# Kernel tuning notes

Hardware: AMD Instinct MI355X
Metric: run time of the kernel (lower is better)

Reference implementation:

```python
import jax, jax.numpy as jnp
import numpy as np

G, S, M = 4, 2048, 1024   # groups (batch), tokens per group, emb dim
E, H, K = 8, 4096, 2      # experts, mlp dim, top-k
CAP = int(K * S / E * 1.25)  # expert capacity = 640
AUX_COEF, Z_COEF = 0.01, 0.001


def setup_inputs() -> dict:
    key = jax.random.key(0)
    k1, k2, k3, k4, k5 = jax.random.split(key, 5)
    return {
        "inputs": jax.random.normal(k1, (G, S, M), jnp.float32),
        "paddings": jnp.zeros((G, S), jnp.float32),  # 1.0 = padded token
        "router_w": jax.random.normal(k2, (M, E), jnp.float32) / np.sqrt(M),
        "wi_gate": jax.random.normal(k3, (E, M, H), jnp.float32) / np.sqrt(M),
        "wi_0": jax.random.normal(k4, (E, M, H), jnp.float32) / np.sqrt(M),
        "wo": jax.random.normal(k5, (E, H, M), jnp.float32) / np.sqrt(H),
    }


def reference(inputs, paddings, router_w, wi_gate, wi_0, wo):
    # Router
    logits = jnp.einsum('gsm,me->gse', inputs, router_w)          # [G,S,E]
    probs = jax.nn.softmax(logits, axis=-1)
    top_p, top_i = jax.lax.top_k(probs, K)                        # [G,S,K]

    nonpad = 1.0 - paddings                                       # [G,S]
    exp_mask = jax.nn.one_hot(top_i, E, dtype=jnp.float32)        # [G,S,K,E]
    exp_mask = exp_mask * nonpad[:, :, None, None]

    # Position in expert (capacity-limited), priority by token order then k slot
    mask_flat = exp_mask.reshape(G, S * K, E)
    pos = jnp.cumsum(mask_flat, axis=1) * mask_flat               # 1-indexed where assigned
    keep = mask_flat * (pos <= CAP)
    pos_oh = jax.nn.one_hot((pos - 1.0).astype(jnp.int32), CAP, dtype=jnp.float32)  # [G,SK,E,CAP]
    dispatch_k = (keep[..., None] * pos_oh).reshape(G, S, K, E, CAP)
    dispatch = dispatch_k.sum(axis=2)                             # [G,S,E,CAP]
    combine = jnp.einsum('gsk,gskec->gsec', top_p, dispatch_k)    # [G,S,E,CAP]

    # Dispatch -> gated expert FFN -> combine
    expert_in = jnp.einsum('gsec,gsm->egcm', dispatch, inputs)    # [E,G,CAP,M]
    h = jax.nn.silu(jnp.einsum('egcm,emh->egch', expert_in, wi_gate)) \
        * jnp.einsum('egcm,emh->egch', expert_in, wi_0)           # [E,G,CAP,H]
    expert_out = jnp.einsum('egch,ehm->egcm', h, wo)              # [E,G,CAP,M]
    output = jnp.einsum('gsec,egcm->gsm', combine, expert_out)    # [G,S,M]

    # Aux losses: load-balancing (Switch style) + router z-loss
    em = jnp.max(jax.nn.one_hot(top_i, E, dtype=jnp.float32), axis=-2)       # [G,S,E]
    lb = jnp.mean(jnp.mean(em, axis=-2) * jnp.mean(probs, axis=-2)) * E * E
    z = jnp.mean(jax.nn.logsumexp(logits, axis=-1) ** 2)
    aux_loss = AUX_COEF * lb + Z_COEF * z
    return output, aux_loss
```

## Files before the change

### kernel.cpp

```cpp
#include <hip/hip_runtime.h>
#include <hip/hip_bf16.h>
#include <math.h>

#define G 4
#define S 2048
#define MDIM 1024
#define E 8
#define HDIM 4096
#define TOPK 2
#define CAP 640
#define GC (G*CAP)

typedef __attribute__((ext_vector_type(8))) short bf16x8;
typedef __attribute__((ext_vector_type(4))) short s16x4;
typedef __attribute__((ext_vector_type(4))) float f32x4;
typedef unsigned int u32;
typedef unsigned short u16;

#define MFMA16(a,b,c) __builtin_amdgcn_mfma_f32_16x16x32_bf16(a,b,c,0,0,0)

__device__ __forceinline__ u16 f2bf(float f) {
    union { float f; u32 u; } v; v.f = f;
    u32 r = v.u + 0x7fffu + ((v.u >> 16) & 1u);
    return (u16)(r >> 16);
}

__device__ __forceinline__ void gload16(const char* gp, char* lp) {
    __builtin_amdgcn_global_load_lds((const __attribute__((address_space(1))) u32*)gp,
                                     (__attribute__((address_space(3))) u32*)lp,
                                     16, 0, 0);
}

__device__ __forceinline__ int swzb(int r) { return ((r >> 1) & 3) << 4; }

__global__ __launch_bounds__(256) void transpose_cvt(const float* __restrict__ in,
                                                     u16* __restrict__ out, int R, int C) {
    int e = blockIdx.z;
    const float* ine = in + (size_t)e * R * C;
    u16* oute = out + (size_t)e * R * C;
    __shared__ float tile[64][68];
    int t = threadIdx.x;
    int x0 = blockIdx.x * 64, y0 = blockIdx.y * 64;
    int lx = (t & 15) * 4, ly = t >> 4;
    #pragma unroll
    for (int i = 0; i < 4; ++i) {
        f32x4 v = *(const f32x4*)(ine + (size_t)(y0 + ly + i * 16) * C + x0 + lx);
        *(f32x4*)&tile[ly + i * 16][lx] = v;
    }
    __syncthreads();
    int rr0 = (t & 15) * 4, cb = t >> 4;
    #pragma unroll
    for (int p = 0; p < 4; ++p) {
        int cc = cb + p * 16;
        s16x4 pk;
        #pragma unroll
        for (int j = 0; j < 4; ++j) pk[j] = (short)f2bf(tile[rr0 + j][cc]);
        *(s16x4*)(oute + (size_t)(x0 + cc) * R + y0 + rr0) = pk;
    }
}

__global__ __launch_bounds__(256) void router_kernel(const float* __restrict__ inp,
                                                     const float* __restrict__ rw,
                                                     int* __restrict__ top_i,
                                                     float* __restrict__ top_p,
                                                     float* __restrict__ partials) {
    int wid = threadIdx.x >> 6, lane = threadIdx.x & 63;
    int tok = blockIdx.x * 4 + wid;
    const float* x = inp + (size_t)tok * MDIM;
    float acc[E] = {0.f,0.f,0.f,0.f,0.f,0.f,0.f,0.f};
    #pragma unroll
    for (int rep = 0; rep < 4; ++rep) {
        int m0 = rep * 256 + lane * 4;
        f32x4 xv = *(const f32x4*)(x + m0);
        #pragma unroll
        for (int j = 0; j < 4; ++j) {
            const float* r = rw + (size_t)(m0 + j) * E;
            float xj = xv[j];
            #pragma unroll
            for (int e = 0; e < E; ++e) acc[e] += xj * r[e];
        }
    }
    #pragma unroll
    for (int e = 0; e < E; ++e)
        #pragma unroll
        for (int off = 32; off; off >>= 1) acc[e] += __shfl_down(acc[e], off);

    __shared__ float part[4][17];
    if (lane == 0) {
        float mx = acc[0];
        #pragma unroll
        for (int e = 1; e < E; ++e) mx = fmaxf(mx, acc[e]);
        float p[E], sum = 0.f;
        #pragma unroll
        for (int e = 0; e < E; ++e) { p[e] = expf(acc[e] - mx); sum += p[e]; }
        float inv = 1.f / sum;
        #pragma unroll
        for (int e = 0; e < E; ++e) p[e] *= inv;
        float lse = logf(sum) + mx;
        int i0 = 0;
        #pragma unroll
        for (int e = 1; e < E; ++e) if (acc[e] > acc[i0]) i0 = e;
        int i1 = (i0 == 0) ? 1 : 0;
        #pragma unroll
        for (int e = 0; e < E; ++e) if (e != i0 && acc[e] > acc[i1]) i1 = e;
        top_i[tok*2+0] = i0; top_i[tok*2+1] = i1;
        top_p[tok*2+0] = p[i0]; top_p[tok*2+1] = p[i1];
        #pragma unroll
        for (int e = 0; e < E; ++e) { part[wid][e] = p[e]; part[wid][8+e] = 0.f; }
        part[wid][8+i0] = 1.f; part[wid][8+i1] = 1.f;
        part[wid][16] = lse * lse;
    }
    __syncthreads();
    if (threadIdx.x < 17) {
        float v = part[0][threadIdx.x] + part[1][threadIdx.x] +
                  part[2][threadIdx.x] + part[3][threadIdx.x];
        partials[(size_t)blockIdx.x * 17 + threadIdx.x] = v;
    }
}

__global__ __launch_bounds__(256) void reduce_partials(const float* __restrict__ partials,
                                                       float* __restrict__ sums) {
    int g = blockIdx.x, t = threadIdx.x;
    float loc[17];
    #pragma unroll
    for (int c = 0; c < 17; ++c) loc[c] = 0.f;
    for (int r = t; r < 1024; r += 256) {
        const float* pr = partials + ((size_t)g * 1024 + r) * 17;
        #pragma unroll
        for (int c = 0; c < 17; ++c) loc[c] += pr[c];
    }
    __shared__ float red[256];
    for (int c = 0; c < 17; ++c) {
        red[t] = loc[c]; __syncthreads();
        for (int off = 128; off; off >>= 1) {
            if (t < off) red[t] += red[t + off];
            __syncthreads();
        }
        if (t == 0) sums[g * 17 + c] = red[0];
        __syncthreads();
    }
}

__global__ void aux_final(const float* __restrict__ sums, float* __restrict__ out) {
    float lb = 0.f, z = 0.f;
    for (int g = 0; g < G; ++g) {
        for (int e = 0; e < E; ++e)
            lb += (sums[g*17 + 8 + e] / (float)S) * (sums[g*17 + e] / (float)S);
        z += sums[g*17 + 16];
    }
    lb = lb / (float)(G * E) * (float)(E * E);
    z /= (float)(G * S);
    out[(size_t)G * S * MDIM] = 0.01f * lb + 0.001f * z;
}

__global__ __launch_bounds__(256) void scan_kernel(const int* __restrict__ top_i,
                                                   const float* __restrict__ pad,
                                                   int* __restrict__ slot_token,
                                                   int* __restrict__ token_c) {
    int b = blockIdx.x; int g = b >> 3, e = b & 7;
    int t = threadIdx.x;
    __shared__ int sums[256];
    int base = t * 16;
    int run = 0; unsigned mask16 = 0; int loc[16];
    #pragma unroll
    for (int j = 0; j < 16; ++j) {
        int i = base + j; int s = i >> 1, k = i & 1;
        int ex = top_i[((size_t)(g * S + s)) * 2 + k];
        int m = (ex == e) && (pad[g * S + s] == 0.f);
        run += m; loc[j] = run; mask16 |= ((unsigned)m << j);
    }
    sums[t] = run; __syncthreads();
    for (int off = 1; off < 256; off <<= 1) {
        int v = (t >= off) ? sums[t - off] : 0;
        __syncthreads();
        sums[t] += v;
        __syncthreads();
    }
    int excl = sums[t] - run;
    #pragma unroll
    for (int j = 0; j < 16; ++j) {
        if ((mask16 >> j) & 1u) {
            int pos = excl + loc[j];
            if (pos <= CAP) {
                int i = base + j; int s = i >> 1, k = i & 1;
                slot_token[((size_t)(e * G + g)) * CAP + (pos - 1)] = s;
                token_c[((size_t)(g * S + s)) * 2 + k] = pos - 1;
            }
        }
    }
}

__global__ __launch_bounds__(128) void gather_kernel(const float* __restrict__ inp,
                                                     const int* __restrict__ slot_token,
                                                     u16* __restrict__ X) {
    int row = blockIdx.x;
    int t = threadIdx.x;
    int s = slot_token[row];
    int g = (row % GC) / CAP;
    bf16x8 v;
    if (s >= 0) {
        const float* src = inp + ((size_t)(g * S + s)) * MDIM + t * 8;
        f32x4 a = *(const f32x4*)src;
        f32x4 b = *(const f32x4*)(src + 4);
        #pragma unroll
        for (int j = 0; j < 4; ++j) { v[j] = (short)f2bf(a[j]); v[4+j] = (short)f2bf(b[j]); }
    } else {
        #pragma unroll
        for (int j = 0; j < 8; ++j) v[j] = 0;
    }
    *(bf16x8*)(X + (size_t)row * MDIM + t * 8) = v;
}

__global__ __launch_bounds__(256, 2) void gemm_ffn12_v6(
        const u16* __restrict__ Xb, const u16* __restrict__ WgT,
        const u16* __restrict__ W0T, u16* __restrict__ Hb) {
    extern __shared__ char smem[];
    const int NK = MDIM / 32;
    int bid = blockIdx.x;
    int swz = (bid & 7) * 640 + (bid >> 3);
    int mt = swz % 20, nt = (swz / 20) % 32, e = swz / 640;
    const char* A  = (const char*)(Xb  + (size_t)e * GC * MDIM   + (size_t)mt * 128 * MDIM);
    const char* Bg = (const char*)(WgT + (size_t)e * HDIM * MDIM + (size_t)nt * 128 * MDIM);
    const char* B0 = (const char*)(W0T + (size_t)e * HDIM * MDIM + (size_t)nt * 128 * MDIM);
    int tid = threadIdx.x, w = tid >> 6, l = tid & 63;
    int wm = w >> 1, wn = w & 1;
    int rl = l >> 2, cch = (l & 3) * 16;
    int fr = l & 15, fg = l >> 4;
    int lswz = ((fr >> 1) & 3) << 4;

    int r0 = 0 * 64 + w * 16 + rl, r1 = 1 * 64 + w * 16 + rl;
    const char* gA0 = A  + (size_t)r0 * MDIM * 2 + (cch ^ swzb(r0));
    const char* gA1 = A  + (size_t)r1 * MDIM * 2 + (cch ^ swzb(r1));
    const char* gG0 = Bg + (size_t)r0 * MDIM * 2 + (cch ^ swzb(r0));
    const char* gG1 = Bg + (size_t)r1 * MDIM * 2 + (cch ^ swzb(r1));
    const char* gO0 = B0 + (size_t)r0 * MDIM * 2 + (cch ^ swzb(r0));
    const char* gO1 = B0 + (size_t)r1 * MDIM * 2 + (cch ^ swzb(r1));
    int baseA = (wm * 64 + fr) * 64 + ((fg * 16) ^ lswz);
    int baseB = (wn * 64 + fr) * 64 + ((fg * 16) ^ lswz);

    f32x4 ag[4][4], ao[4][4];
    #pragma unroll
    for (int i = 0; i < 4; ++i)
        #pragma unroll
        for (int j = 0; j < 4; ++j) { ag[i][j] = (f32x4){0,0,0,0}; ao[i][j] = (f32x4){0,0,0,0}; }

    auto stage = [&](int tt) {
        int kk = tt * 64;
        char* dst = smem + (tt & 1) * 24576;
        gload16(gA0 + kk, dst + 0 * 4096 + w * 1024);
        gload16(gA1 + kk, dst + 1 * 4096 + w * 1024);
        gload16(gG0 + kk, dst + 8192 + 0 * 4096 + w * 1024);
        gload16(gG1 + kk, dst + 8192 + 1 * 4096 + w * 1024);
        gload16(gO0 + kk, dst + 16384 + 0 * 4096 + w * 1024);
        gload16(gO1 + kk, dst + 16384 + 1 * 4096 + w * 1024);
    };

    stage(0);
    asm volatile("s_waitcnt vmcnt(0)" ::: "memory");
    __builtin_amdgcn_s_barrier();

    #pragma unroll 1
    for (int t = 0; t < NK; ++t) {
        if (t + 1 < NK) stage(t + 1);
        const char* bufc = smem + (t & 1) * 24576;
        bf16x8 af[4], bg_[4], bo_[4];
        #pragma unroll
        for (int fm = 0; fm < 4; ++fm) af[fm]  = *(const bf16x8*)(bufc + baseA + fm * 1024);
        #pragma unroll
        for (int fn = 0; fn < 4; ++fn) bg_[fn] = *(const bf16x8*)(bufc + 8192  + baseB + fn * 1024);
        #pragma unroll
        for (int fn = 0; fn < 4; ++fn) bo_[fn] = *(const bf16x8*)(bufc + 16384 + baseB + fn * 1024);
        __builtin_amdgcn_s_setprio(1);
        #pragma unroll
        for (int fm = 0; fm < 4; ++fm)
            #pragma unroll
            for (int fn = 0; fn < 4; ++fn) {
                ag[fm][fn] = MFMA16(bg_[fn], af[fm], ag[fm][fn]);
                ao[fm][fn] = MFMA16(bo_[fn], af[fm], ao[fm][fn]);
            }
        __builtin_amdgcn_s_setprio(0);
        asm volatile("s_waitcnt vmcnt(0)" ::: "memory");
        __builtin_amdgcn_s_barrier();
    }

    u16* He = Hb + (size_t)e * GC * HDIM;
    int row0 = mt * 128 + wm * 64 + fr;
    int col0 = nt * 128 + wn * 64 + fg * 4;
    #pragma unroll
    for (int fm = 0; fm < 4; ++fm)
        #pragma unroll
        for (int fn = 0; fn < 4; ++fn) {
            s16x4 pk;
            #pragma unroll
            for (int r = 0; r < 4; ++r) {
                float gv = ag[fm][fn][r], ov = ao[fm][fn][r];
                float hv = gv / (1.f + __expf(-gv)) * ov;
                pk[r] = (short)f2bf(hv);
            }
            *(s16x4*)(He + (size_t)(row0 + fm * 16) * HDIM + col0 + fn * 16) = pk;
        }
}

__global__ __launch_bounds__(256, 2) void gemm_out_v6(
        const u16* __restrict__ Hb, const u16* __restrict__ WoT,
        float* __restrict__ EO) {
    extern __shared__ char smem[];
    const int NK = HDIM / 32;
    int bid = blockIdx.x;
    int swz = (bid & 7) * 80 + (bid >> 3);
    int mt = swz % 20, nt = (swz / 20) & 3, e = swz / 80;
    const char* A = (const char*)(Hb  + (size_t)e * GC * HDIM   + (size_t)mt * 128 * HDIM);
    const char* B = (const char*)(WoT + (size_t)e * MDIM * HDIM + (size_t)nt * 256 * HDIM);
    int tid = threadIdx.x, w = tid >> 6, l = tid & 63;
    int wm = w >> 1, wn = w & 1;
    int rl = l >> 2, cch = (l & 3) * 16;
    int fr = l & 15, fg = l >> 4;
    int lswz = ((fr >> 1) & 3) << 4;

    int r0 = 0 * 64 + w * 16 + rl, r1 = 1 * 64 + w * 16 + rl;
    int r2 = 2 * 64 + w * 16 + rl, r3 = 3 * 64 + w * 16 + rl;
    const char* gA0 = A + (size_t)r0 * HDIM * 2 + (cch ^ swzb(r0));
    const char* gA1 = A + (size_t)r1 * HDIM * 2 + (cch ^ swzb(r1));
    const char* gB0 = B + (size_t)r0 * HDIM * 2 + (cch ^ swzb(r0));
    const char* gB1 = B + (size_t)r1 * HDIM * 2 + (cch ^ swzb(r1));
    const char* gB2 = B + (size_t)r2 * HDIM * 2 + (cch ^ swzb(r2));
    const char* gB3 = B + (size_t)r3 * HDIM * 2 + (cch ^ swzb(r3));
    int baseA = (wm * 64  + fr) * 64 + ((fg * 16) ^ lswz);
    int baseB = (wn * 128 + fr) * 64 + ((fg * 16) ^ lswz);

    f32x4 acc[4][8];
    #pragma unroll
    for (int i = 0; i < 4; ++i)
        #pragma unroll
        for (int j = 0; j < 8; ++j) acc[i][j] = (f32x4){0,0,0,0};

    auto stage = [&](int tt) {
        int kk = tt * 64;
        char* dst = smem + (tt & 1) * 24576;
        gload16(gA0 + kk, dst + 0 * 4096 + w * 1024);
        gload16(gA1 + kk, dst + 1 * 4096 + w * 1024);
        gload16(gB0 + kk, dst + 8192 + 0 * 4096 + w * 1024);
        gload16(gB1 + kk, dst + 8192 + 1 * 4096 + w * 1024);
        gload16(gB2 + kk, dst + 8192 + 2 * 4096 + w * 1024);
        gload16(gB3 + kk, dst + 8192 + 3 * 4096 + w * 1024);
    };

    stage(0);
    asm volatile("s_waitcnt vmcnt(0)" ::: "memory");
    __builtin_amdgcn_s_barrier();

    #pragma unroll 1
    for (int t = 0; t < NK; ++t) {
        if (t + 1 < NK) stage(t + 1);
        const char* bufc = smem + (t & 1) * 24576;
        bf16x8 af[4], bf[8];
        #pragma unroll
        for (int fm = 0; fm < 4; ++fm) af[fm] = *(const bf16x8*)(bufc + baseA + fm * 1024);
        #pragma unroll
        for (int fn = 0; fn < 8; ++fn) bf[fn] = *(const bf16x8*)(bufc + 8192 + baseB + fn * 1024);
        __builtin_amdgcn_s_setprio(1);
        #pragma unroll
        for (int fm = 0; fm < 4; ++fm)
            #pragma unroll
            for (int fn = 0; fn < 8; ++fn)
                acc[fm][fn] = MFMA16(bf[fn], af[fm], acc[fm][fn]);
        __builtin_amdgcn_s_setprio(0);
        asm volatile("s_waitcnt vmcnt(0)" ::: "memory");
        __builtin_amdgcn_s_barrier();
    }

    float* Ee = EO + (size_t)e * GC * MDIM;
    int row0 = mt * 128 + wm * 64 + fr;
    int col0 = nt * 256 + wn * 128 + fg * 4;
    #pragma unroll
    for (int fm = 0; fm < 4; ++fm)
        #pragma unroll
        for (int fn = 0; fn < 8; ++fn)
            *(f32x4*)(Ee + (size_t)(row0 + fm * 16) * MDIM + col0 + fn * 16) = acc[fm][fn];
}

__global__ __launch_bounds__(256) void combine_kernel(const float* __restrict__ EO,
                                                      const int* __restrict__ top_i,
                                                      const float* __restrict__ top_p,
                                                      const int* __restrict__ token_c,
                                                      float* __restrict__ out) {
    int tok = blockIdx.x, t = threadIdx.x;
    int g = tok >> 11;
    f32x4 acc = {0.f, 0.f, 0.f, 0.f};
    #pragma unroll
    for (int k = 0; k < 2; ++k) {
        int c = token_c[tok * 2 + k];
        if (c >= 0) {
            int e = top_i[tok * 2 + k];
            float p = top_p[tok * 2 + k];
            const float* src = EO + ((size_t)e * GC + g * CAP + c) * MDIM + t * 4;
            f32x4 v = *(const f32x4*)src;
            #pragma unroll
            for (int j = 0; j < 4; ++j) acc[j] += p * v[j];
        }
    }
    *(f32x4*)(out + (size_t)tok * MDIM + t * 4) = acc;
}

extern "C" void kernel_launch(void* const* d_in, const int* in_sizes, int n_in,
                              void* d_out, int out_size, void* d_ws, size_t ws_size,
                              hipStream_t stream) {
    (void)in_sizes; (void)n_in; (void)out_size; (void)ws_size;
    const float* inputs   = (const float*)d_in[0];
    const float* paddings = (const float*)d_in[1];
    const float* router_w = (const float*)d_in[2];
    const float* wi_gate  = (const float*)d_in[3];
    const float* wi_0     = (const float*)d_in[4];
    const float* wo       = (const float*)d_in[5];
    float* out = (float*)d_out;

    char* p = (char*)d_ws;
    u16* WgT = (u16*)p; p += (size_t)E * HDIM * MDIM * 2;
    u16* W0T = (u16*)p; p += (size_t)E * HDIM * MDIM * 2;
    u16* WoT = (u16*)p; p += (size_t)E * HDIM * MDIM * 2;
    u16* Xb  = (u16*)p; p += (size_t)E * GC * MDIM * 2;
    u16* Hb  = (u16*)p; p += (size_t)E * GC * HDIM * 2;
    float* EO = (float*)p; p += (size_t)E * GC * MDIM * 4;
    int*   top_i = (int*)p;   p += (size_t)G * S * TOPK * 4;
    float* top_p = (float*)p; p += (size_t)G * S * TOPK * 4;
    int*   token_c = (int*)p; p += (size_t)G * S * TOPK * 4;
    int*   slot_token = (int*)p; p += (size_t)E * G * CAP * 4;
    float* partials = (float*)p; p += (size_t)4096 * 17 * 4;
    float* sums = (float*)p; p += 4 * 17 * 4;

    hipMemsetAsync(token_c, 0xFF, (size_t)G * S * TOPK * 4, stream);
    hipMemsetAsync(slot_token, 0xFF, (size_t)E * G * CAP * 4, stream);

    hipFuncSetAttribute((const void*)gemm_ffn12_v6,
                        hipFuncAttributeMaxDynamicSharedMemorySize, 49152);
    hipFuncSetAttribute((const void*)gemm_out_v6,
                        hipFuncAttributeMaxDynamicSharedMemorySize, 49152);

    transpose_cvt<<<dim3(HDIM/64, MDIM/64, E), 256, 0, stream>>>(wi_gate, WgT, MDIM, HDIM);
    transpose_cvt<<<dim3(HDIM/64, MDIM/64, E), 256, 0, stream>>>(wi_0,   W0T, MDIM, HDIM);
    transpose_cvt<<<dim3(MDIM/64, HDIM/64, E), 256, 0, stream>>>(wo,     WoT, HDIM, MDIM);

    router_kernel<<<G * S / 4, 256, 0, stream>>>(inputs, router_w, top_i, top_p, partials);
    reduce_partials<<<G, 256, 0, stream>>>(partials, sums);
    scan_kernel<<<G * E, 256, 0, stream>>>(top_i, paddings, slot_token, token_c);
    gather_kernel<<<E * GC, 128, 0, stream>>>(inputs, slot_token, Xb);
    gemm_ffn12_v6<<<5120, 256, 49152, stream>>>(Xb, WgT, W0T, Hb);
    gemm_out_v6<<<640, 256, 49152, stream>>>(Hb, WoT, EO);
    combine_kernel<<<G * S, 256, 0, stream>>>(EO, top_i, top_p, token_c, out);
    aux_final<<<1, 1, 0, stream>>>(sums, out);
}
```

Measured before the change: 802.8 us.

## Retile expert GEMMs to 512-thread blocks with 32x32x16 MFMA and K=64 stages

Both expert FFN GEMMs move from 256-thread blocks using 16x16x32 MFMA with K=32 LDS stages to 512-thread blocks using 32x32x16 MFMA with K=64 stages and a wider 128-byte XOR swizzle. The gate/up GEMM also grows its M tile from 128 to 256 rows, halving the grid and increasing reuse of weight tiles. The aim is fewer barriers per unit of work, fewer LDS reads per MFMA flop, and better operand reuse. In exchange, each block uses more LDS (up to 128 KB) and runs at one block per CU, which lowers occupancy and may reduce latency hiding.

```diff
diff --git a/kernel.cpp b/kernel.cpp
--- a/kernel.cpp
+++ b/kernel.cpp
@@ -14,10 +14,12 @@
 typedef __attribute__((ext_vector_type(8))) short bf16x8;
 typedef __attribute__((ext_vector_type(4))) short s16x4;
 typedef __attribute__((ext_vector_type(4))) float f32x4;
+typedef __attribute__((ext_vector_type(16))) float f32x16;
 typedef unsigned int u32;
 typedef unsigned short u16;
 
-#define MFMA16(a,b,c) __builtin_amdgcn_mfma_f32_16x16x32_bf16(a,b,c,0,0,0)
+#define MFMA32(a,b,c) __builtin_amdgcn_mfma_f32_32x32x16_bf16(a,b,c,0,0,0)
+#define BAR() __builtin_amdgcn_s_barrier()
 
 __device__ __forceinline__ u16 f2bf(float f) {
     union { float f; u32 u; } v; v.f = f;
@@ -31,7 +33,7 @@
                                      16, 0, 0);
 }
 
-__device__ __forceinline__ int swzb(int r) { return ((r >> 1) & 3) << 4; }
+__device__ __forceinline__ int swz128(int r) { return ((r >> 1) & 7) << 4; }
 
 __global__ __launch_bounds__(256) void transpose_cvt(const float* __restrict__ in,
                                                      u16* __restrict__ out, int R, int C) {
@@ -211,172 +213,212 @@
     *(bf16x8*)(X + (size_t)row * MDIM + t * 8) = v;
 }
 
-__global__ __launch_bounds__(256, 2) void gemm_ffn12_v6(
+__global__ __launch_bounds__(512, 1) void gemm_ffn12_v9(
         const u16* __restrict__ Xb, const u16* __restrict__ WgT,
         const u16* __restrict__ W0T, u16* __restrict__ Hb) {
     extern __shared__ char smem[];
-    const int NK = MDIM / 32;
+    const int NK = MDIM / 64;
     int bid = blockIdx.x;
-    int swz = (bid & 7) * 640 + (bid >> 3);
-    int mt = swz % 20, nt = (swz / 20) % 32, e = swz / 640;
-    const char* A  = (const char*)(Xb  + (size_t)e * GC * MDIM   + (size_t)mt * 128 * MDIM);
+    int swz = (bid & 7) * 320 + (bid >> 3);
+    int mt = swz % 10, nt = (swz / 10) & 31, e = swz / 320;
+    const char* A  = (const char*)(Xb  + (size_t)e * GC * MDIM   + (size_t)mt * 256 * MDIM);
     const char* Bg = (const char*)(WgT + (size_t)e * HDIM * MDIM + (size_t)nt * 128 * MDIM);
     const char* B0 = (const char*)(W0T + (size_t)e * HDIM * MDIM + (size_t)nt * 128 * MDIM);
     int tid = threadIdx.x, w = tid >> 6, l = tid & 63;
-    int wm = w >> 1, wn = w & 1;
-    int rl = l >> 2, cch = (l & 3) * 16;
-    int fr = l & 15, fg = l >> 4;
-    int lswz = ((fr >> 1) & 3) << 4;
-
-    int r0 = 0 * 64 + w * 16 + rl, r1 = 1 * 64 + w * 16 + rl;
-    const char* gA0 = A  + (size_t)r0 * MDIM * 2 + (cch ^ swzb(r0));
-    const char* gA1 = A  + (size_t)r1 * MDIM * 2 + (cch ^ swzb(r1));
-    const char* gG0 = Bg + (size_t)r0 * MDIM * 2 + (cch ^ swzb(r0));
-    const char* gG1 = Bg + (size_t)r1 * MDIM * 2 + (cch ^ swzb(r1));
-    const char* gO0 = B0 + (size_t)r0 * MDIM * 2 + (cch ^ swzb(r0));
-    const char* gO1 = B0 + (size_t)r1 * MDIM * 2 + (cch ^ swzb(r1));
-    int baseA = (wm * 64 + fr) * 64 + ((fg * 16) ^ lswz);
-    int baseB = (wn * 64 + fr) * 64 + ((fg * 16) ^ lswz);
-
-    f32x4 ag[4][4], ao[4][4];
-    #pragma unroll
-    for (int i = 0; i < 4; ++i)
-        #pragma unroll
-        for (int j = 0; j < 4; ++j) { ag[i][j] = (f32x4){0,0,0,0}; ao[i][j] = (f32x4){0,0,0,0}; }
+    int wm = w >> 2, wn = w & 3;
+    int lr = l & 31, lk = l >> 5;
+    int lswz = ((lr >> 1) & 7) << 4;
+
+    int koff[4];
+    #pragma unroll
+    for (int ks = 0; ks < 4; ++ks) koff[ks] = (ks * 32 + lk * 16) ^ lswz;
+    int baseA[4];
+    #pragma unroll
+    for (int rb = 0; rb < 4; ++rb) baseA[rb] = (wm * 128 + rb * 32 + lr) * 128;
+    int baseB = (wn * 32 + lr) * 128;
+
+    const char* srcA[4]; const char* srcG[2]; const char* srcO[2];
+    #pragma unroll
+    for (int p = 0; p < 4; ++p) {
+        int gr = p * 64 + w * 8 + (l >> 3);
+        srcA[p] = A + (size_t)gr * (MDIM * 2) + (((l & 7) * 16) ^ swz128(gr));
+    }
+    #pragma unroll
+    for (int p = 0; p < 2; ++p) {
+        int gr = p * 64 + w * 8 + (l >> 3);
+        srcG[p] = Bg + (size_t)gr * (MDIM * 2) + (((l & 7) * 16) ^ swz128(gr));
+        srcO[p] = B0 + (size_t)gr * (MDIM * 2) + (((l & 7) * 16) ^ swz128(gr));
+    }
+
+    f32x16 zz;
+    #pragma unroll
+    for (int i = 0; i < 16; ++i) zz[i] = 0.f;
+    f32x16 ag[4], ao[4];
+    #pragma unroll
+    for (int rb = 0; rb < 4; ++rb) { ag[rb] = zz; ao[rb] = zz; }
 
     auto stage = [&](int tt) {
-        int kk = tt * 64;
-        char* dst = smem + (tt & 1) * 24576;
-        gload16(gA0 + kk, dst + 0 * 4096 + w * 1024);
-        gload16(gA1 + kk, dst + 1 * 4096 + w * 1024);
-        gload16(gG0 + kk, dst + 8192 + 0 * 4096 + w * 1024);
-        gload16(gG1 + kk, dst + 8192 + 1 * 4096 + w * 1024);
-        gload16(gO0 + kk, dst + 16384 + 0 * 4096 + w * 1024);
-        gload16(gO1 + kk, dst + 16384 + 1 * 4096 + w * 1024);
+        int kk = tt * 128;
+        char* dst = smem + (tt & 1) * 65536;
+        #pragma unroll
+        for (int p = 0; p < 4; ++p)
+            gload16(srcA[p] + kk, dst + (p * 64 + w * 8) * 128);
+        #pragma unroll
+        for (int p = 0; p < 2; ++p) {
+            gload16(srcG[p] + kk, dst + 32768 + (p * 64 + w * 8) * 128);
+            gload16(srcO[p] + kk, dst + 49152 + (p * 64 + w * 8) * 128);
+        }
     };
 
     stage(0);
     asm volatile("s_waitcnt vmcnt(0)" ::: "memory");
-    __builtin_amdgcn_s_barrier();
+    BAR();
 
     #pragma unroll 1
     for (int t = 0; t < NK; ++t) {
         if (t + 1 < NK) stage(t + 1);
-        const char* bufc = smem + (t & 1) * 24576;
-        bf16x8 af[4], bg_[4], bo_[4];
-        #pragma unroll
-        for (int fm = 0; fm < 4; ++fm) af[fm]  = *(const bf16x8*)(bufc + baseA + fm * 1024);
-        #pragma unroll
-        for (int fn = 0; fn < 4; ++fn) bg_[fn] = *(const bf16x8*)(bufc + 8192  + baseB + fn * 1024);
-        #pragma unroll
-        for (int fn = 0; fn < 4; ++fn) bo_[fn] = *(const bf16x8*)(bufc + 16384 + baseB + fn * 1024);
-        __builtin_amdgcn_s_setprio(1);
-        #pragma unroll
-        for (int fm = 0; fm < 4; ++fm)
-            #pragma unroll
-            for (int fn = 0; fn < 4; ++fn) {
-                ag[fm][fn] = MFMA16(bg_[fn], af[fm], ag[fm][fn]);
-                ao[fm][fn] = MFMA16(bo_[fn], af[fm], ao[fm][fn]);
+        const char* bufc = smem + (t & 1) * 65536;
+        #pragma unroll
+        for (int ks = 0; ks < 4; ++ks) {
+            bf16x8 bg = *(const bf16x8*)(bufc + 32768 + baseB + koff[ks]);
+            bf16x8 bo = *(const bf16x8*)(bufc + 49152 + baseB + koff[ks]);
+            bf16x8 af[4];
+            #pragma unroll
+            for (int rb = 0; rb < 4; ++rb)
+                af[rb] = *(const bf16x8*)(bufc + baseA[rb] + koff[ks]);
+            __builtin_amdgcn_s_setprio(1);
+            #pragma unroll
+            for (int rb = 0; rb < 4; ++rb) {
+                ag[rb] = MFMA32(bg, af[rb], ag[rb]);
+                ao[rb] = MFMA32(bo, af[rb], ao[rb]);
             }
-        __builtin_amdgcn_s_setprio(0);
+            __builtin_amdgcn_s_setprio(0);
+        }
         asm volatile("s_waitcnt vmcnt(0)" ::: "memory");
-        __builtin_amdgcn_s_barrier();
+        BAR();
     }
 
     u16* He = Hb + (size_t)e * GC * HDIM;
-    int row0 = mt * 128 + wm * 64 + fr;
-    int col0 = nt * 128 + wn * 64 + fg * 4;
-    #pragma unroll
-    for (int fm = 0; fm < 4; ++fm)
-        #pragma unroll
-        for (int fn = 0; fn < 4; ++fn) {
+    int row0 = mt * 256 + wm * 128 + lr;
+    int col0 = nt * 128 + wn * 32 + lk * 4;
+    #pragma unroll
+    for (int rb = 0; rb < 4; ++rb) {
+        size_t rowoff = (size_t)(row0 + rb * 32) * HDIM;
+        #pragma unroll
+        for (int q = 0; q < 4; ++q) {
             s16x4 pk;
             #pragma unroll
             for (int r = 0; r < 4; ++r) {
-                float gv = ag[fm][fn][r], ov = ao[fm][fn][r];
+                float gv = ag[rb][q * 4 + r], ov = ao[rb][q * 4 + r];
                 float hv = gv / (1.f + __expf(-gv)) * ov;
                 pk[r] = (short)f2bf(hv);
             }
-            *(s16x4*)(He + (size_t)(row0 + fm * 16) * HDIM + col0 + fn * 16) = pk;
-        }
-}
-
-__global__ __launch_bounds__(256, 2) void gemm_out_v6(
+            *(s16x4*)(He + rowoff + col0 + q * 8) = pk;
+        }
+    }
+}
+
+__global__ __launch_bounds__(512, 1) void gemm_out_v9(
         const u16* __restrict__ Hb, const u16* __restrict__ WoT,
         float* __restrict__ EO) {
     extern __shared__ char smem[];
-    const int NK = HDIM / 32;
+    const int NK = HDIM / 64;
     int bid = blockIdx.x;
     int swz = (bid & 7) * 80 + (bid >> 3);
-    int mt = swz % 20, nt = (swz / 20) & 3, e = swz / 80;
+    int nt = swz & 3, mt = (swz / 4) % 20, e = swz / 80;
     const char* A = (const char*)(Hb  + (size_t)e * GC * HDIM   + (size_t)mt * 128 * HDIM);
     const char* B = (const char*)(WoT + (size_t)e * MDIM * HDIM + (size_t)nt * 256 * HDIM);
     int tid = threadIdx.x, w = tid >> 6, l = tid & 63;
-    int wm = w >> 1, wn = w & 1;
-    int rl = l >> 2, cch = (l & 3) * 16;
-    int fr = l & 15, fg = l >> 4;
-    int lswz = ((fr >> 1) & 3) << 4;
-
-    int r0 = 0 * 64 + w * 16 + rl, r1 = 1 * 64 + w * 16 + rl;
-    int r2 = 2 * 64 + w * 16 + rl, r3 = 3 * 64 + w * 16 + rl;
-    const char* gA0 = A + (size_t)r0 * HDIM * 2 + (cch ^ swzb(r0));
-    const char* gA1 = A + (size_t)r1 * HDIM * 2 + (cch ^ swzb(r1));
-    const char* gB0 = B + (size_t)r0 * HDIM * 2 + (cch ^ swzb(r0));
-    const char* gB1 = B + (size_t)r1 * HDIM * 2 + (cch ^ swzb(r1));
-    const char* gB2 = B + (size_t)r2 * HDIM * 2 + (cch ^ swzb(r2));
-    const char* gB3 = B + (size_t)r3 * HDIM * 2 + (cch ^ swzb(r3));
-    int baseA = (wm * 64  + fr) * 64 + ((fg * 16) ^ lswz);
-    int baseB = (wn * 128 + fr) * 64 + ((fg * 16) ^ lswz);
-
-    f32x4 acc[4][8];
-    #pragma unroll
-    for (int i = 0; i < 4; ++i)
-        #pragma unroll
-        for (int j = 0; j < 8; ++j) acc[i][j] = (f32x4){0,0,0,0};
+    int wm = w >> 2, wn = w & 3;
+    int lr = l & 31, lk = l >> 5;
+    int lswz = ((lr >> 1) & 7) << 4;
+
+    int koff[4];
+    #pragma unroll
+    for (int ks = 0; ks < 4; ++ks) koff[ks] = (ks * 32 + lk * 16) ^ lswz;
+    int baseA[2], baseB[2];
+    #pragma unroll
+    for (int rb = 0; rb < 2; ++rb) baseA[rb] = (wm * 64 + rb * 32 + lr) * 128;
+    #pragma unroll
+    for (int cb = 0; cb < 2; ++cb) baseB[cb] = (wn * 64 + cb * 32 + lr) * 128;
+
+    const char* srcA[2]; const char* srcB[4];
+    #pragma unroll
+    for (int p = 0; p < 2; ++p) {
+        int gr = p * 64 + w * 8 + (l >> 3);
+        srcA[p] = A + (size_t)gr * (HDIM * 2) + (((l & 7) * 16) ^ swz128(gr));
+    }
+    #pragma unroll
+    for (int p = 0; p < 4; ++p) {
+        int gr = p * 64 + w * 8 + (l >> 3);
+        srcB[p] = B + (size_t)gr * (HDIM * 2) + (((l & 7) * 16) ^ swz128(gr));
+    }
+
+    f32x16 zz;
+    #pragma unroll
+    for (int i = 0; i < 16; ++i) zz[i] = 0.f;
+    f32x16 acc[2][2];
+    #pragma unroll
+    for (int i = 0; i < 2; ++i)
+        #pragma unroll
+        for (int j = 0; j < 2; ++j) acc[i][j] = zz;
 
     auto stage = [&](int tt) {
-        int kk = tt * 64;
-        char* dst = smem + (tt & 1) * 24576;
-        gload16(gA0 + kk, dst + 0 * 4096 + w * 1024);
-        gload16(gA1 + kk, dst + 1 * 4096 + w * 1024);
-        gload16(gB0 + kk, dst + 8192 + 0 * 4096 + w * 1024);
-        gload16(gB1 + kk, dst + 8192 + 1 * 4096 + w * 1024);
-        gload16(gB2 + kk, dst + 8192 + 2 * 4096 + w * 1024);
-        gload16(gB3 + kk, dst + 8192 + 3 * 4096 + w * 1024);
+        int kk = tt * 128;
+        char* dst = smem + (tt & 1) * 49152;
+        #pragma unroll
+        for (int p = 0; p < 2; ++p)
+            gload16(srcA[p] + kk, dst + (p * 64 + w * 8) * 128);
+        #pragma unroll
+        for (int p = 0; p < 4; ++p)
+            gload16(srcB[p] + kk, dst + 16384 + (p * 64 + w * 8) * 128);
     };
 
     stage(0);
     asm volatile("s_waitcnt vmcnt(0)" ::: "memory");
-    __builtin_amdgcn_s_barrier();
+    BAR();
 
     #pragma unroll 1
     for (int t = 0; t < NK; ++t) {
         if (t + 1 < NK) stage(t + 1);
-        const char* bufc = smem + (t & 1) * 24576;
-        bf16x8 af[4], bf[8];
-        #pragma unroll
-        for (int fm = 0; fm < 4; ++fm) af[fm] = *(const bf16x8*)(bufc + baseA + fm * 1024);
-        #pragma unroll
-        for (int fn = 0; fn < 8; ++fn) bf[fn] = *(const bf16x8*)(bufc + 8192 + baseB + fn * 1024);
-        __builtin_amdgcn_s_setprio(1);
-        #pragma unroll
-        for (int fm = 0; fm < 4; ++fm)
-            #pragma unroll
-            for (int fn = 0; fn < 8; ++fn)
-                acc[fm][fn] = MFMA16(bf[fn], af[fm], acc[fm][fn]);
-        __builtin_amdgcn_s_setprio(0);
+        const char* bufc = smem + (t & 1) * 49152;
+        #pragma unroll
+        for (int ks = 0; ks < 4; ++ks) {
+            bf16x8 bf[2], af[2];
+            #pragma unroll
+            for (int cb = 0; cb < 2; ++cb)
+                bf[cb] = *(const bf16x8*)(bufc + 16384 + baseB[cb] + koff[ks]);
+            #pragma unroll
+            for (int rb = 0; rb < 2; ++rb)
+                af[rb] = *(const bf16x8*)(bufc + baseA[rb] + koff[ks]);
+            __builtin_amdgcn_s_setprio(1);
+            #pragma unroll
+            for (int rb = 0; rb < 2; ++rb)
+                #pragma unroll
+                for (int cb = 0; cb < 2; ++cb)
+                    acc[rb][cb] = MFMA32(bf[cb], af[rb], acc[rb][cb]);
+            __builtin_amdgcn_s_setprio(0);
+        }
         asm volatile("s_waitcnt vmcnt(0)" ::: "memory");
-        __builtin_amdgcn_s_barrier();
+        BAR();
     }
 
     float* Ee = EO + (size_t)e * GC * MDIM;
-    int row0 = mt * 128 + wm * 64 + fr;
-    int col0 = nt * 256 + wn * 128 + fg * 4;
-    #pragma unroll
-    for (int fm = 0; fm < 4; ++fm)
-        #pragma unroll
-        for (int fn = 0; fn < 8; ++fn)
-            *(f32x4*)(Ee + (size_t)(row0 + fm * 16) * MDIM + col0 + fn * 16) = acc[fm][fn];
+    int row0 = mt * 128 + wm * 64 + lr;
+    int col0 = nt * 256 + wn * 64 + lk * 4;
+    #pragma unroll
+    for (int rb = 0; rb < 2; ++rb) {
+        size_t rowoff = (size_t)(row0 + rb * 32) * MDIM;
+        #pragma unroll
+        for (int cb = 0; cb < 2; ++cb)
+            #pragma unroll
+            for (int q = 0; q < 4; ++q) {
+                f32x4 v;
+                #pragma unroll
+                for (int r = 0; r < 4; ++r) v[r] = acc[rb][cb][q * 4 + r];
+                *(f32x4*)(Ee + rowoff + col0 + cb * 32 + q * 8) = v;
+            }
+    }
 }
 
 __global__ __launch_bounds__(256) void combine_kernel(const float* __restrict__ EO,
@@ -431,10 +473,10 @@
     hipMemsetAsync(token_c, 0xFF, (size_t)G * S * TOPK * 4, stream);
     hipMemsetAsync(slot_token, 0xFF, (size_t)E * G * CAP * 4, stream);
 
-    hipFuncSetAttribute((const void*)gemm_ffn12_v6,
-                        hipFuncAttributeMaxDynamicSharedMemorySize, 49152);
-    hipFuncSetAttribute((const void*)gemm_out_v6,
-                        hipFuncAttributeMaxDynamicSharedMemorySize, 49152);
+    hipFuncSetAttribute((const void*)gemm_ffn12_v9,
+                        hipFuncAttributeMaxDynamicSharedMemorySize, 131072);
+    hipFuncSetAttribute((const void*)gemm_out_v9,
+                        hipFuncAttributeMaxDynamicSharedMemorySize, 98304);
 
     transpose_cvt<<<dim3(HDIM/64, MDIM/64, E), 256, 0, stream>>>(wi_gate, WgT, MDIM, HDIM);
     transpose_cvt<<<dim3(HDIM/64, MDIM/64, E), 256, 0, stream>>>(wi_0,   W0T, MDIM, HDIM);
@@ -444,8 +486,8 @@
     reduce_partials<<<G, 256, 0, stream>>>(partials, sums);
     scan_kernel<<<G * E, 256, 0, stream>>>(top_i, paddings, slot_token, token_c);
     gather_kernel<<<E * GC, 128, 0, stream>>>(inputs, slot_token, Xb);
-    gemm_ffn12_v6<<<5120, 256, 49152, stream>>>(Xb, WgT, W0T, Hb);
-    gemm_out_v6<<<640, 256, 49152, stream>>>(Hb, WoT, EO);
+    gemm_ffn12_v9<<<2560, 512, 131072, stream>>>(Xb, WgT, W0T, Hb);
+    gemm_out_v9<<<640, 512, 98304, stream>>>(Hb, WoT, EO);
     combine_kernel<<<G * S, 256, 0, stream>>>(EO, top_i, top_p, token_c, out);
     aux_final<<<1, 1, 0, stream>>>(sums, out);
 }
```

New measurement: 787.7 us. About the same (-1.9%).
